# Performance work log

Measured on AMD Instinct MI355X. Metric: run time of the kernel, lower is better.

Reference implementation:

```python
import jax, jax.numpy as jnp
import numpy as np

ALPHA = 0.9        # synaptic decay (hidden layers; layer 0 uses 0*syn + h)
BETA = 0.85        # membrane leak
THRESHOLD = 1.0
SIM_TIME = 50
SCALE = 100.0      # SurrGradSpike.scale


@jax.custom_vjp
def spike_fn(x):
    # Heaviside step: 1.0 where x > 0 (strict, matching torch `input > 0`)
    return (x > 0).astype(x.dtype)

def _spike_fwd(x):
    return spike_fn(x), x

def _spike_bwd(x, g):
    # normalized fast-sigmoid surrogate gradient (Zenke & Ganguli 2018)
    return (g / (SCALE * jnp.abs(x) + 1.0) ** 2,)

spike_fn.defvjp(_spike_fwd, _spike_bwd)


def setup_inputs() -> dict:
    key = jax.random.key(0)
    k0, k1, k2, k3 = jax.random.split(key, 4)
    return {
        "inputs": jax.random.normal(k0, (128, 1024), dtype=jnp.float32),
        "W0": jax.random.normal(k1, (1024, 2048), dtype=jnp.float32),
        "W1": jax.random.normal(k2, (2048, 2048), dtype=jnp.float32),
        "W2": jax.random.normal(k3, (2048, 512), dtype=jnp.float32),
    }


def _dsnn_forward(inputs, weights):
    batch = inputs.shape[0]
    n_layers = len(weights)
    syn0 = tuple(jnp.zeros((batch, W.shape[1]), dtype=inputs.dtype) for W in weights)
    mem0 = tuple(jnp.zeros((batch, W.shape[1]), dtype=inputs.dtype) for W in weights)

    def step(carry, _):
        syn, mem = carry
        new_syn, new_mem = [], []
        prev_spk = None
        for l, W in enumerate(weights):
            # feedforward drive: static input at layer 0, current-step spikes after
            h = inputs @ W if l == 0 else prev_spk @ W
            # layer 0: new_syn = 0*syn + h ; others: alpha*syn + h
            s = h if l == 0 else ALPHA * syn[l] + h
            m = BETA * mem[l] + s
            mthr = m - THRESHOLD
            out = spike_fn(mthr)
            if l < n_layers - 1:
                # hard reset to 0 where spiked (output layer never resets)
                m = jnp.where(mthr > 0, jnp.zeros_like(m), m)
            prev_spk = out
            new_syn.append(s)
            new_mem.append(m)
        return (tuple(new_syn), tuple(new_mem)), None

    (syn, mem), _ = jax.lax.scan(step, (syn0, mem0), None, length=SIM_TIME)
    # torch returns mem_rec[-1][-1]: output-layer membrane at final timestep
    return mem[-1]


def reference(inputs, W0, W1, W2):
    return _dsnn_forward(inputs, (W0, W1, W2))
```

## Files before the change

### kernel.cpp

```cpp
#include <hip/hip_runtime.h>

#define ALPHA 0.9f
#define BETA  0.85f
#define TSIM  50
#define BATCH 128
#define N0    1024
#define N1    2048
#define N2    2048
#define N3    512

#define A50   0.00515379f
#define B50   0.000295764f
#define INVAB 20.0f

__global__ __launch_bounds__(256) void gemm_f32_splitk(const float* __restrict__ A,
                                                       const float* __restrict__ B,
                                                       float* __restrict__ Cp,
                                                       int M, int N, int K, int KC) {
    __shared__ float As[16][65];
    __shared__ float Bs[16][68];

    const int tid = threadIdx.x;
    const int tx  = tid % 16;
    const int ty  = tid / 16;
    const int bx  = blockIdx.x;
    const int by  = blockIdx.y;
    const int z   = blockIdx.z;

    float acc[4][4] = {};

    const int ar = tid / 4;
    const int ak = (tid % 4) * 4;
    const int br = tid / 16;
    const int bc = (tid % 16) * 4;

    const int kbeg = z * KC;
    for (int k0 = kbeg; k0 < kbeg + KC; k0 += 16) {
        float4 av = *(const float4*)&A[(size_t)(by * 64 + ar) * K + k0 + ak];
        As[ak + 0][ar] = av.x;
        As[ak + 1][ar] = av.y;
        As[ak + 2][ar] = av.z;
        As[ak + 3][ar] = av.w;
        float4 bv = *(const float4*)&B[(size_t)(k0 + br) * N + bx * 64 + bc];
        *(float4*)&Bs[br][bc] = bv;
        __syncthreads();

#pragma unroll
        for (int kk = 0; kk < 16; ++kk) {
            float a0 = As[kk][ty * 4 + 0];
            float a1 = As[kk][ty * 4 + 1];
            float a2 = As[kk][ty * 4 + 2];
            float a3 = As[kk][ty * 4 + 3];
            float b0 = Bs[kk][tx * 4 + 0];
            float b1 = Bs[kk][tx * 4 + 1];
            float b2 = Bs[kk][tx * 4 + 2];
            float b3 = Bs[kk][tx * 4 + 3];
            acc[0][0] += a0 * b0; acc[0][1] += a0 * b1; acc[0][2] += a0 * b2; acc[0][3] += a0 * b3;
            acc[1][0] += a1 * b0; acc[1][1] += a1 * b1; acc[1][2] += a1 * b2; acc[1][3] += a1 * b3;
            acc[2][0] += a2 * b0; acc[2][1] += a2 * b1; acc[2][2] += a2 * b2; acc[2][3] += a2 * b3;
            acc[3][0] += a3 * b0; acc[3][1] += a3 * b1; acc[3][2] += a3 * b2; acc[3][3] += a3 * b3;
        }
        __syncthreads();
    }

#pragma unroll
    for (int i = 0; i < 4; ++i) {
        float4 v = make_float4(acc[i][0], acc[i][1], acc[i][2], acc[i][3]);
        *(float4*)&Cp[((size_t)z * M + by * 64 + ty * 4 + i) * N + bx * 64 + tx * 4] = v;
    }
}

__global__ __launch_bounds__(256) void scan_l0_classify(const float* __restrict__ P0,
                                                        float* __restrict__ C0,
                                                        int* __restrict__ jlist0,
                                                        unsigned long long* __restrict__ mask0,
                                                        int* __restrict__ count0) {
    const int b     = blockIdx.x;
    const int chunk = blockIdx.y;
    const int tid   = threadIdx.x;
    const int j     = chunk * 256 + tid;
    const int lane  = tid & 63;
    const int wv    = tid >> 6;

    float h = 0.f;
#pragma unroll
    for (int z = 0; z < 8; ++z) h += P0[((size_t)z * BATCH + b) * N1 + j];

    float m = 0.f;
    unsigned long long mask = 0ull;
#pragma unroll
    for (int t = 0; t < TSIM; ++t) {
        m = BETA * m + h;
        if (m - 1.f > 0.f) { mask |= (1ull << t); m = 0.f; }
    }
    const unsigned long long FULL = (1ull << TSIM) - 1ull;
    C0[(size_t)b * N1 + j] = (mask == FULL) ? 1.f : 0.f;

    const bool has = (mask != 0ull) && (mask != FULL);
    const unsigned long long bal = __ballot(has);

    __shared__ int wcnt[4];
    if (lane == 0) wcnt[wv] = __popcll(bal);
    __syncthreads();
    int base = 0;
#pragma unroll
    for (int w = 0; w < 4; ++w)
        if (w < wv) base += wcnt[w];
    const int pos = base + __popcll(bal & ((1ull << lane) - 1ull));

    const size_t lbase = (size_t)(b * 8 + chunk) * 256;
    if (has) {
        jlist0[lbase + pos] = j;
        mask0[lbase + pos]  = mask;
    }
    if (tid == 0) count0[b * 8 + chunk] = wcnt[0] + wcnt[1] + wcnt[2] + wcnt[3];
}

__global__ __launch_bounds__(256) void h1_scan_a2(const float* __restrict__ PB1,
                                                  const float* __restrict__ W1,
                                                  const int* __restrict__ jlist0,
                                                  const unsigned long long* __restrict__ mask0,
                                                  const int* __restrict__ count0,
                                                  float* __restrict__ A2) {
    const int b  = blockIdx.x;
    const int jc = blockIdx.y * 256 + threadIdx.x;

    float base = 0.f;
#pragma unroll
    for (int z = 0; z < 8; ++z) base += PB1[((size_t)z * BATCH + b) * N2 + jc];

    float corr[TSIM];
#pragma unroll
    for (int t = 0; t < TSIM; ++t) corr[t] = 0.f;

    for (int c = 0; c < 8; ++c) {
        const int cnt      = count0[b * 8 + c];
        const size_t lbase = (size_t)(b * 8 + c) * 256;
        for (int e = 0; e < cnt; ++e) {
            const int j                 = jlist0[lbase + e];
            const unsigned long long mk = mask0[lbase + e];
            const float w               = W1[(size_t)j * N2 + jc];
            const unsigned lo = (unsigned)mk, hi = (unsigned)(mk >> 32);
#pragma unroll
            for (int t = 0; t < 32; ++t)
                if ((lo >> t) & 1u) corr[t] += w;
#pragma unroll
            for (int t = 32; t < TSIM; ++t)
                if ((hi >> (t - 32)) & 1u) corr[t] += w;
        }
    }

    float s = 0.f, m = 0.f, a2 = 0.f;
    float pa = A50, pb = B50;
    const float inva = 1.0f / ALPHA, invb = 1.0f / BETA;
#pragma unroll
    for (int t = 0; t < TSIM; ++t) {
        s = ALPHA * s + (base + corr[t]);
        m = BETA * m + s;
        if (m - 1.f > 0.f) {
            a2 += (pa - pb) * INVAB;
            m = 0.f;
        }
        pa *= inva;
        pb *= invb;
    }
    A2[(size_t)b * N2 + jc] = a2;
}

__global__ __launch_bounds__(256) void reduce_out(const float* __restrict__ PB2,
                                                  float* __restrict__ out) {
    const int idx = blockIdx.x * 256 + threadIdx.x;
    float v = 0.f;
#pragma unroll
    for (int z = 0; z < 16; ++z) v += PB2[(size_t)z * (BATCH * N3) + idx];
    out[idx] = v;
}

extern "C" void kernel_launch(void* const* d_in, const int* in_sizes, int n_in,
                              void* d_out, int out_size, void* d_ws, size_t ws_size,
                              hipStream_t stream) {
    const float* inputs = (const float*)d_in[0];
    const float* W0     = (const float*)d_in[1];
    const float* W1     = (const float*)d_in[2];
    const float* W2     = (const float*)d_in[3];
    float* out = (float*)d_out;

    float* P0  = (float*)d_ws;
    float* C0  = P0 + 8 * BATCH * N1;
    float* PB1 = C0 + BATCH * N1;
    float* A2  = PB1 + 8 * BATCH * N2;
    float* PB2 = A2 + BATCH * N2;
    int* jl0   = (int*)(PB2 + 16 * BATCH * N3);
    int* cnt0  = jl0 + BATCH * N1;
    unsigned long long* mk0 = (unsigned long long*)(cnt0 + 1024);

    gemm_f32_splitk<<<dim3(N1 / 64, BATCH / 64, 8), 256, 0, stream>>>(
        inputs, W0, P0, BATCH, N1, N0, N0 / 8);

    scan_l0_classify<<<dim3(BATCH, N1 / 256), 256, 0, stream>>>(P0, C0, jl0, mk0, cnt0);

    gemm_f32_splitk<<<dim3(N2 / 64, BATCH / 64, 8), 256, 0, stream>>>(
        C0, W1, PB1, BATCH, N2, N1, N1 / 8);

    h1_scan_a2<<<dim3(BATCH, N2 / 256), 256, 0, stream>>>(
        PB1, W1, jl0, mk0, cnt0, A2);

    gemm_f32_splitk<<<dim3(N3 / 64, BATCH / 64, 16), 256, 0, stream>>>(
        A2, W2, PB2, BATCH, N3, N2, N2 / 16);

    reduce_out<<<(BATCH * N3) / 256, 256, 0, stream>>>(PB2, out);
}
```

Before: 164.2 us.

## Use bf16 hi/lo split MFMA for layer-1 GEMM and two-phase corr scan

Adds a per-call kernel that transposes W1 and splits it into bf16 high and low parts, then computes the C0·W1 GEMM with bf16 MFMA instructions (two MFMAs per tile, one per part), using 16-way split-K and direct global-to-LDS loads. C0 is binary, so it is stored exactly as bf16. The h1_scan_a2 kernel now processes the 50 timesteps in two phases of 25, so the per-thread corr array is half the size and register pressure drops, at the cost of walking the sparse spike list twice. The extra transpose pass reads all of W1 and writes 16 MB of bf16 every call, and the hi/lo split gives only about 16 mantissa bits.

```diff
diff --git a/kernel.cpp b/kernel.cpp
--- a/kernel.cpp
+++ b/kernel.cpp
@@ -1,4 +1,5 @@
 #include <hip/hip_runtime.h>
+#include <hip/hip_bf16.h>
 
 #define ALPHA 0.9f
 #define BETA  0.85f
@@ -12,6 +13,12 @@
 #define A50   0.00515379f
 #define B50   0.000295764f
 #define INVAB 20.0f
+
+typedef __attribute__((ext_vector_type(8))) short bf16x8;
+typedef __attribute__((ext_vector_type(4))) float f32x4;
+
+#define GLOBAL_AS __attribute__((address_space(1)))
+#define LDS_AS    __attribute__((address_space(3)))
 
 __global__ __launch_bounds__(256) void gemm_f32_splitk(const float* __restrict__ A,
                                                        const float* __restrict__ B,
@@ -70,8 +77,126 @@
     }
 }
 
+__global__ __launch_bounds__(256) void split_transpose(const float* __restrict__ W,
+                                                       __hip_bfloat16* __restrict__ Th,
+                                                       __hip_bfloat16* __restrict__ Tl,
+                                                       int K, int N) {
+    __shared__ float tile[32][33];
+    const int tx = threadIdx.x % 32;
+    const int ty = threadIdx.x / 32;
+    const int k0 = blockIdx.y * 32;
+    const int n0 = blockIdx.x * 32;
+
+#pragma unroll
+    for (int i = 0; i < 4; ++i)
+        tile[ty + i * 8][tx] = W[(size_t)(k0 + ty + i * 8) * N + n0 + tx];
+    __syncthreads();
+
+#pragma unroll
+    for (int i = 0; i < 4; ++i) {
+        const float w = tile[tx][ty + i * 8];
+        const __hip_bfloat16 hi = __float2bfloat16(w);
+        const float lo = w - __bfloat162float(hi);
+        const size_t o = (size_t)(n0 + ty + i * 8) * K + k0 + tx;
+        Th[o] = hi;
+        Tl[o] = __float2bfloat16(lo);
+    }
+}
+
+template <int BN, int WGM, int WGN, int WMT, int WNT>
+__global__ __launch_bounds__(256) void gemm_bf16_split_k(const __hip_bfloat16* __restrict__ A,
+                                                         const __hip_bfloat16* __restrict__ Bh,
+                                                         const __hip_bfloat16* __restrict__ Bl,
+                                                         float* __restrict__ Cp,
+                                                         int M, int N, int K, int KC) {
+    constexpr int BM = 128;
+    constexpr int BK = 32;
+    constexpr int NA = (BM * BK) / (256 * 8);
+    constexpr int NB = (BN * BK) / (256 * 8);
+
+    __shared__ alignas(16) __hip_bfloat16 As[BM * BK];
+    __shared__ alignas(16) __hip_bfloat16 Bhs[BN * BK];
+    __shared__ alignas(16) __hip_bfloat16 Bls[BN * BK];
+
+    const int tid  = threadIdx.x;
+    const int wave = tid >> 6;
+    const int lane = tid & 63;
+    const int quad = lane >> 4;
+    const int l16  = lane & 15;
+
+    const int m0 = blockIdx.y * BM;
+    const int n0 = blockIdx.x * BN;
+    const int z  = blockIdx.z;
+
+    const int wm = (wave % WGM) * (WMT * 16);
+    const int wn = (wave / WGM) * (WNT * 16);
+
+    f32x4 acc[WMT][WNT] = {};
+
+    const __hip_bfloat16* agp[NA];
+    int aoff[NA];
+#pragma unroll
+    for (int i = 0; i < NA; ++i) {
+        const int c = i * 256 + tid;
+        agp[i]  = A + (size_t)(m0 + (c >> 2)) * K + (c & 3) * 8;
+        aoff[i] = c * 8;
+    }
+    const __hip_bfloat16 *bhgp[NB], *blgp[NB];
+    int boff[NB];
+#pragma unroll
+    for (int i = 0; i < NB; ++i) {
+        const int c = i * 256 + tid;
+        bhgp[i] = Bh + (size_t)(n0 + (c >> 2)) * K + (c & 3) * 8;
+        blgp[i] = Bl + (size_t)(n0 + (c >> 2)) * K + (c & 3) * 8;
+        boff[i] = c * 8;
+    }
+
+    const int kbeg = z * KC;
+    for (int k0 = kbeg; k0 < kbeg + KC; k0 += BK) {
+#pragma unroll
+        for (int i = 0; i < NA; ++i)
+            __builtin_amdgcn_global_load_lds((const GLOBAL_AS void*)(agp[i] + k0),
+                                             (LDS_AS void*)&As[aoff[i]], 16, 0, 0);
+#pragma unroll
+        for (int i = 0; i < NB; ++i) {
+            __builtin_amdgcn_global_load_lds((const GLOBAL_AS void*)(bhgp[i] + k0),
+                                             (LDS_AS void*)&Bhs[boff[i]], 16, 0, 0);
+            __builtin_amdgcn_global_load_lds((const GLOBAL_AS void*)(blgp[i] + k0),
+                                             (LDS_AS void*)&Bls[boff[i]], 16, 0, 0);
+        }
+        __syncthreads();
+
+        bf16x8 af[WMT], bhf[WNT], blf[WNT];
+#pragma unroll
+        for (int i = 0; i < WMT; ++i)
+            af[i] = *(const bf16x8*)&As[(wm + i * 16 + l16) * BK + quad * 8];
+#pragma unroll
+        for (int j = 0; j < WNT; ++j) {
+            bhf[j] = *(const bf16x8*)&Bhs[(wn + j * 16 + l16) * BK + quad * 8];
+            blf[j] = *(const bf16x8*)&Bls[(wn + j * 16 + l16) * BK + quad * 8];
+        }
+#pragma unroll
+        for (int i = 0; i < WMT; ++i)
+#pragma unroll
+            for (int j = 0; j < WNT; ++j) {
+                acc[i][j] = __builtin_amdgcn_mfma_f32_16x16x32_bf16(af[i], bhf[j], acc[i][j], 0, 0, 0);
+                acc[i][j] = __builtin_amdgcn_mfma_f32_16x16x32_bf16(af[i], blf[j], acc[i][j], 0, 0, 0);
+            }
+        __syncthreads();
+    }
+
+#pragma unroll
+    for (int i = 0; i < WMT; ++i)
+#pragma unroll
+        for (int j = 0; j < WNT; ++j)
+#pragma unroll
+            for (int r = 0; r < 4; ++r)
+                Cp[((size_t)z * M + m0 + wm + i * 16 + quad * 4 + r) * N + n0 + wn + j * 16 + l16] =
+                    acc[i][j][r];
+}
+
 __global__ __launch_bounds__(256) void scan_l0_classify(const float* __restrict__ P0,
-                                                        float* __restrict__ C0,
+                                                        __hip_bfloat16* __restrict__ C0,
                                                         int* __restrict__ jlist0,
                                                         unsigned long long* __restrict__ mask0,
                                                         int* __restrict__ count0) {
@@ -94,7 +219,7 @@
         if (m - 1.f > 0.f) { mask |= (1ull << t); m = 0.f; }
     }
     const unsigned long long FULL = (1ull << TSIM) - 1ull;
-    C0[(size_t)b * N1 + j] = (mask == FULL) ? 1.f : 0.f;
+    C0[(size_t)b * N1 + j] = __float2bfloat16((mask == FULL) ? 1.f : 0.f);
 
     const bool has = (mask != 0ull) && (mask != FULL);
     const unsigned long long bal = __ballot(has);
@@ -127,42 +252,45 @@
 
     float base = 0.f;
 #pragma unroll
-    for (int z = 0; z < 8; ++z) base += PB1[((size_t)z * BATCH + b) * N2 + jc];
-
-    float corr[TSIM];
-#pragma unroll
-    for (int t = 0; t < TSIM; ++t) corr[t] = 0.f;
-
-    for (int c = 0; c < 8; ++c) {
-        const int cnt      = count0[b * 8 + c];
-        const size_t lbase = (size_t)(b * 8 + c) * 256;
-        for (int e = 0; e < cnt; ++e) {
-            const int j                 = jlist0[lbase + e];
-            const unsigned long long mk = mask0[lbase + e];
-            const float w               = W1[(size_t)j * N2 + jc];
-            const unsigned lo = (unsigned)mk, hi = (unsigned)(mk >> 32);
-#pragma unroll
-            for (int t = 0; t < 32; ++t)
-                if ((lo >> t) & 1u) corr[t] += w;
-#pragma unroll
-            for (int t = 32; t < TSIM; ++t)
-                if ((hi >> (t - 32)) & 1u) corr[t] += w;
-        }
-    }
+    for (int z = 0; z < 16; ++z) base += PB1[((size_t)z * BATCH + b) * N2 + jc];
 
     float s = 0.f, m = 0.f, a2 = 0.f;
     float pa = A50, pb = B50;
     const float inva = 1.0f / ALPHA, invb = 1.0f / BETA;
-#pragma unroll
-    for (int t = 0; t < TSIM; ++t) {
-        s = ALPHA * s + (base + corr[t]);
-        m = BETA * m + s;
-        if (m - 1.f > 0.f) {
-            a2 += (pa - pb) * INVAB;
-            m = 0.f;
-        }
-        pa *= inva;
-        pb *= invb;
+
+    float corr[25];
+
+#pragma unroll
+    for (int phase = 0; phase < 2; ++phase) {
+        const int shift = phase * 25;
+
+#pragma unroll
+        for (int t = 0; t < 25; ++t) corr[t] = 0.f;
+
+        for (int c = 0; c < 8; ++c) {
+            const int cnt      = count0[b * 8 + c];
+            const size_t lbase = (size_t)(b * 8 + c) * 256;
+            for (int e = 0; e < cnt; ++e) {
+                const unsigned mk = (unsigned)(mask0[lbase + e] >> shift);
+                const int j       = jlist0[lbase + e];
+                const float w     = W1[(size_t)j * N2 + jc];
+#pragma unroll
+                for (int t = 0; t < 25; ++t)
+                    if ((mk >> t) & 1u) corr[t] += w;
+            }
+        }
+
+#pragma unroll
+        for (int t = 0; t < 25; ++t) {
+            s = ALPHA * s + (base + corr[t]);
+            m = BETA * m + s;
+            if (m - 1.f > 0.f) {
+                a2 += (pa - pb) * INVAB;
+                m = 0.f;
+            }
+            pa *= inva;
+            pb *= invb;
+        }
     }
     A2[(size_t)b * N2 + jc] = a2;
 }
@@ -186,21 +314,26 @@
     float* out = (float*)d_out;
 
     float* P0  = (float*)d_ws;
-    float* C0  = P0 + 8 * BATCH * N1;
-    float* PB1 = C0 + BATCH * N1;
-    float* A2  = PB1 + 8 * BATCH * N2;
+    float* PB1 = P0 + 8 * BATCH * N1;
+    float* A2  = PB1 + 16 * BATCH * N2;
     float* PB2 = A2 + BATCH * N2;
-    int* jl0   = (int*)(PB2 + 16 * BATCH * N3);
-    int* cnt0  = jl0 + BATCH * N1;
-    unsigned long long* mk0 = (unsigned long long*)(cnt0 + 1024);
+    unsigned long long* mk0 = (unsigned long long*)(PB2 + 16 * BATCH * N3);
+    __hip_bfloat16* C0bf = (__hip_bfloat16*)(mk0 + BATCH * 8 * 256);
+    __hip_bfloat16* W1th = C0bf + (size_t)BATCH * N1;
+    __hip_bfloat16* W1tl = W1th + (size_t)N2 * N1;
+    int* jl0  = (int*)(W1tl + (size_t)N2 * N1);
+    int* cnt0 = jl0 + BATCH * 8 * 256;
+
+    split_transpose<<<dim3(N2 / 32, N1 / 32), 256, 0, stream>>>(W1, W1th, W1tl, N1, N2);
 
     gemm_f32_splitk<<<dim3(N1 / 64, BATCH / 64, 8), 256, 0, stream>>>(
         inputs, W0, P0, BATCH, N1, N0, N0 / 8);
 
-    scan_l0_classify<<<dim3(BATCH, N1 / 256), 256, 0, stream>>>(P0, C0, jl0, mk0, cnt0);
-
-    gemm_f32_splitk<<<dim3(N2 / 64, BATCH / 64, 8), 256, 0, stream>>>(
-        C0, W1, PB1, BATCH, N2, N1, N1 / 8);
+    scan_l0_classify<<<dim3(BATCH, N1 / 256), 256, 0, stream>>>(P0, C0bf, jl0, mk0, cnt0);
+
+    gemm_bf16_split_k<128, 2, 2, 4, 4>
+        <<<dim3(N2 / 128, BATCH / 128, 16), 256, 0, stream>>>(
+            C0bf, W1th, W1tl, PB1, BATCH, N2, N1, N1 / 16);
 
     h1_scan_a2<<<dim3(BATCH, N2 / 256), 256, 0, stream>>>(
         PB1, W1, jl0, mk0, cnt0, A2);
```

Result: no change. 166.2 us (+1.2%).
